# Kernel tuning notes

Hardware: AMD Instinct MI355X
Metric: run time of the kernel (lower is better)

Reference implementation:

```python
import jax, jax.numpy as jnp
import numpy as np

N, E = 50000, 600000
IN_DIM, HID, OUT_DIM = 128, 256, 64


def _sage_conv(x, edge_index, W_l, W_r, b):
    # PyG SAGEConv (mean aggr, root_weight=True):
    # out = mean_{j in N(i)} x_j @ W_l + x_i @ W_r + b
    src, dst = edge_index[0], edge_index[1]
    msg = x[src]  # [E, d] gather
    agg = jax.ops.segment_sum(msg, dst, num_segments=N)  # [N, d]
    cnt = jax.ops.segment_sum(jnp.ones((E,), dtype=x.dtype), dst, num_segments=N)
    agg = agg / jnp.maximum(cnt, 1.0)[:, None]
    return agg @ W_l + x @ W_r + b


def setup_inputs() -> dict:
    key = jax.random.key(0)
    ks = jax.random.split(key, 8)
    x = jax.random.normal(ks[0], (N, IN_DIM), dtype=jnp.float32)
    edge_index = jax.random.randint(ks[1], (2, E), 0, N, dtype=jnp.int64)
    s1 = 1.0 / np.sqrt(IN_DIM)
    s2 = 1.0 / np.sqrt(HID)
    W1_l = jax.random.uniform(ks[2], (IN_DIM, HID), jnp.float32, -s1, s1)
    W1_r = jax.random.uniform(ks[3], (IN_DIM, HID), jnp.float32, -s1, s1)
    b1 = jnp.zeros((HID,), jnp.float32)
    W2_l = jax.random.uniform(ks[4], (HID, OUT_DIM), jnp.float32, -s2, s2)
    W2_r = jax.random.uniform(ks[5], (HID, OUT_DIM), jnp.float32, -s2, s2)
    b2 = jnp.zeros((OUT_DIM,), jnp.float32)
    return {"x": x, "edge_index": edge_index, "W1_l": W1_l, "W1_r": W1_r,
            "b1": b1, "W2_l": W2_l, "W2_r": W2_r, "b2": b2}


def reference(x, edge_index, W1_l, W1_r, b1, W2_l, W2_r, b2):
    # SAGE.forward, eval mode (dropout = identity)
    h = jax.nn.relu(_sage_conv(x, edge_index, W1_l, W1_r, b1))
    out = _sage_conv(h, edge_index, W2_l, W2_r, b2)
    return out
```

## Files before the change

### kernel.cpp

```cpp
#include <hip/hip_runtime.h>

#define N_NODES 50000
#define N_EDGES 600000
#define N_PAD   50048
#define IN_DIM 128
#define HID 256
#define OUT_DIM 64
#define MAX_DEG 64

typedef __attribute__((ext_vector_type(4))) float f32x4;
typedef __attribute__((ext_vector_type(8))) short short8;
typedef unsigned short u16;
typedef unsigned int u32;

__device__ __forceinline__ float bf2f(u32 lo16) {
  u32 u = lo16 << 16;
  return __builtin_bit_cast(float, u);
}
__device__ __forceinline__ u16 f2bf(float f) {
  u32 u = __builtin_bit_cast(u32, f);
  u = (u + 0x7FFF + ((u >> 16) & 1)) >> 16;
  return (u16)u;
}

#define SEG0 (N_PAD * 16)
#define SEG1 (SEG0 + 128 * 64)
#define SEG2 (SEG1 + 64 * 64)
#define SEG3 (SEG2 + N_NODES)
#define PREP_TOT SEG3

__global__ void k_prep(const float* __restrict__ x,
                       const float* __restrict__ W1l, const float* __restrict__ W1r,
                       const float* __restrict__ W2l, const float* __restrict__ W2r,
                       u16* __restrict__ xb, u16* __restrict__ W1p,
                       u16* __restrict__ W2p, int* __restrict__ cnt) {
  int idx = blockIdx.x * 256 + threadIdx.x;
  if (idx < SEG0) {
    int row = idx >> 4;
    int c8 = (idx & 15) * 8;
    short8 o;
    if (row < N_NODES) {
      f32x4 a = *(const f32x4*)&x[(size_t)row * 128 + c8];
      f32x4 b = *(const f32x4*)&x[(size_t)row * 128 + c8 + 4];
      o[0] = (short)f2bf(a[0]); o[1] = (short)f2bf(a[1]);
      o[2] = (short)f2bf(a[2]); o[3] = (short)f2bf(a[3]);
      o[4] = (short)f2bf(b[0]); o[5] = (short)f2bf(b[1]);
      o[6] = (short)f2bf(b[2]); o[7] = (short)f2bf(b[3]);
    } else {
      for (int j = 0; j < 8; ++j) o[j] = 0;
    }
    *(short8*)&xb[(size_t)row * 128 + c8] = o;
  } else if (idx < SEG1) {
    int i = idx - SEG0;
    int F = i >> 6, l = i & 63;
    int wch = F >> 6, kt = (F >> 4) & 3, kk = (F >> 3) & 1, n = F & 7;
    int row = wch * 128 + n * 16 + (l & 15);
    int kb = kt * 64 + kk * 32 + (l >> 4) * 8;
    short8 o;
#pragma unroll
    for (int j = 0; j < 8; ++j) {
      int k = kb + j;
      float v = (k < 128) ? W1l[(size_t)k * HID + row] : W1r[(size_t)(k - 128) * HID + row];
      o[j] = (short)f2bf(v);
    }
    *(short8*)&W1p[(size_t)i * 8] = o;
  } else if (idx < SEG2) {
    int i = idx - SEG1;
    int G = i >> 6, l = i & 63;
    int wch = G >> 5, kk = (G >> 2) & 7, n = G & 3;
    int row = wch * 64 + n * 16 + (l & 15);
    int kb = kk * 32 + (l >> 4) * 8;
    short8 o;
#pragma unroll
    for (int j = 0; j < 8; ++j) {
      int k = kb + j;
      float v = (row < 64) ? W2l[(size_t)k * OUT_DIM + row]
                           : W2r[(size_t)k * OUT_DIM + (row - 64)];
      o[j] = (short)f2bf(v);
    }
    *(short8*)&W2p[(size_t)i * 8] = o;
  } else if (idx < SEG3) {
    cnt[idx - SEG2] = 0;
  }
}


__global__ void k_fill(const int* __restrict__ src, const int* __restrict__ dst,
                       int* __restrict__ cnt, int* __restrict__ bucket) {
  int e = blockIdx.x * 256 + threadIdx.x;
  if (e < N_EDGES) {
    int d = dst[e];
    int pos = atomicAdd(&cnt[d], 1);
    if (pos < MAX_DEG) bucket[(size_t)d * MAX_DEG + pos] = src[e];
  }
}


__global__ void k_agg(const u16* __restrict__ xb, const int* __restrict__ cnt,
                      const int* __restrict__ bucket, u16* __restrict__ agg) {
  int node = blockIdx.x * 4 + (threadIdx.x >> 6);
  if (node >= N_PAD) return;
  int lane = threadIdx.x & 63;
  int es = lane >> 4, dl = lane & 15;
  int deg = (node < N_NODES) ? cnt[node] : 0;
  int sreg = (node < N_NODES) ? bucket[(size_t)node * MAX_DEG + lane] : 0;
  float acc[8] = {0.f, 0.f, 0.f, 0.f, 0.f, 0.f, 0.f, 0.f};
  short8 pend = (short8){0, 0, 0, 0, 0, 0, 0, 0};
  for (int e = 0; e < deg; e += 4) {
    int ee = e + es;
    int s = __shfl(sreg, ee & 63);
    short8 v = (short8){0, 0, 0, 0, 0, 0, 0, 0};
    if (ee < deg) v = *(const short8*)&xb[(size_t)s * 128 + dl * 8];
#pragma unroll
    for (int j = 0; j < 8; ++j) acc[j] += bf2f((u16)pend[j]);
    pend = v;
  }
#pragma unroll
  for (int j = 0; j < 8; ++j) acc[j] += bf2f((u16)pend[j]);
#pragma unroll
  for (int j = 0; j < 8; ++j) {
    acc[j] += __shfl_xor(acc[j], 16);
    acc[j] += __shfl_xor(acc[j], 32);
  }
  float inv = 1.f / fmaxf((float)deg, 1.f);
  if (es == 0) {
    short8 o;
#pragma unroll
    for (int j = 0; j < 8; ++j) o[j] = (short)f2bf(acc[j] * inv);
    *(short8*)&agg[(size_t)node * 128 + dl * 8] = o;
  }
}


__device__ __forceinline__ void gl_lds16(const void* g, void* l) {
  __builtin_amdgcn_global_load_lds((const __attribute__((address_space(1))) u32*)g,
                                   (__attribute__((address_space(3))) u32*)l, 16, 0, 0);
}

__global__ __launch_bounds__(256, 3) void k_mlp(
    const u16* __restrict__ agg, const u16* __restrict__ xb,
    const u16* __restrict__ W1p, const u16* __restrict__ W2p,
    const float* __restrict__ b1, u16* __restrict__ pb, u16* __restrict__ qb) {
  __shared__ u16 hs[64 * 256];
  __shared__ u16 As[2][64 * 64];
  const int t = threadIdx.x;
  const int wave = t >> 6;
  const int lane = t & 63;
  const int brow = blockIdx.x * 64;
  const int lr = lane & 15;
  const int kg = lane >> 4;
  const int wch = wave & 1;

  const int wr = (wave >> 1) * 32;
  const int wc = wch * 128;

  f32x4 acc[2][8];
#pragma unroll
  for (int m = 0; m < 2; ++m)
#pragma unroll
    for (int n = 0; n < 8; ++n) acc[m][n] = (f32x4){0.f, 0.f, 0.f, 0.f};

  auto stageA = [&](int buf, int kt) {
    const u16* base = (kt < 2) ? agg : xb;
    const int koff = (kt & 1) * 64;
#pragma unroll
    for (int i = 0; i < 2; ++i) {
      int chunk = wave * 2 + i;
      int f = chunk * 1024 + lane * 16;
      int row = f >> 7;
      int cbs = (f & 127) ^ ((row & 7) << 4);
      gl_lds16(&base[(size_t)(brow + row) * 128 + koff + (cbs >> 1)],
               (char*)As[buf] + chunk * 1024);
    }
  };

  stageA(0, 0);
  __syncthreads();

#pragma unroll
  for (int kt = 0; kt < 4; ++kt) {
    const int cur = kt & 1;
    if (kt < 3) stageA(cur ^ 1, kt + 1);
#pragma unroll
    for (int kk = 0; kk < 2; ++kk) {
      short8 af[2], bfr[8];
      const int cb = kk * 64 + kg * 16;
#pragma unroll
      for (int m = 0; m < 2; ++m) {
        int row = wr + m * 16 + lr;
        af[m] = *(const short8*)((const char*)As[cur] + row * 128 + (cb ^ ((row & 7) << 4)));
      }
#pragma unroll
      for (int n = 0; n < 8; ++n)
        bfr[n] = *(const short8*)&W1p[(size_t)(((wch * 4 + kt) * 2 + kk) * 8 + n) * 512 +
                                      lane * 8];
#pragma unroll
      for (int m = 0; m < 2; ++m)
#pragma unroll
        for (int n = 0; n < 8; ++n)
          acc[m][n] =
              __builtin_amdgcn_mfma_f32_16x16x32_bf16(af[m], bfr[n], acc[m][n], 0, 0, 0);
    }
    __syncthreads();
  }

#pragma unroll
  for (int n = 0; n < 8; ++n) {
    int col = wc + n * 16 + lr;
    float bv = b1[col];
#pragma unroll
    for (int m = 0; m < 2; ++m) {
#pragma unroll
      for (int j = 0; j < 4; ++j) {
        int row = wr + kg * 4 + m * 16 + j;
        float v = fmaxf(acc[m][n][j] + bv, 0.f);
        *(u16*)((char*)hs + row * 512 + ((col * 2) ^ ((row & 7) << 4))) = f2bf(v);
      }
    }
  }
  __syncthreads();

  const int wr2 = (wave >> 1) * 32;
  f32x4 acc2[2][4];
#pragma unroll
  for (int m = 0; m < 2; ++m)
#pragma unroll
    for (int n = 0; n < 4; ++n) acc2[m][n] = (f32x4){0.f, 0.f, 0.f, 0.f};

#pragma unroll
  for (int kk = 0; kk < 8; ++kk) {
    const int cb = kk * 64 + kg * 16;
    short8 af[2], bfr[4];
#pragma unroll
    for (int m = 0; m < 2; ++m) {
      int row = wr2 + m * 16 + lr;
      af[m] = *(const short8*)((const char*)hs + row * 512 + (cb ^ ((row & 7) << 4)));
    }
#pragma unroll
    for (int n = 0; n < 4; ++n)
      bfr[n] = *(const short8*)&W2p[(size_t)((wch * 8 + kk) * 4 + n) * 512 + lane * 8];
#pragma unroll
    for (int m = 0; m < 2; ++m)
#pragma unroll
      for (int n = 0; n < 4; ++n)
        acc2[m][n] =
            __builtin_amdgcn_mfma_f32_16x16x32_bf16(af[m], bfr[n], acc2[m][n], 0, 0, 0);
  }

  u16* outb = wch ? qb : pb;
#pragma unroll
  for (int n = 0; n < 4; ++n) {
    int col = n * 16 + lr;
#pragma unroll
    for (int m = 0; m < 2; ++m) {
#pragma unroll
      for (int j = 0; j < 4; ++j) {
        int row = brow + wr2 + kg * 4 + m * 16 + j;
        outb[(size_t)row * 64 + col] = f2bf(acc2[m][n][j]);
      }
    }
  }
}


__global__ void k_out(const u16* __restrict__ pb, const u16* __restrict__ qb,
                      const int* __restrict__ cnt, const int* __restrict__ bucket,
                      const float* __restrict__ b2, float* __restrict__ out) {
  int node = blockIdx.x * 4 + (threadIdx.x >> 6);
  if (node >= N_NODES) return;
  int lane = threadIdx.x & 63;
  int es = lane >> 3, dl = lane & 7;
  int deg = cnt[node];
  int sreg = bucket[(size_t)node * MAX_DEG + lane];
  float acc[8] = {0.f, 0.f, 0.f, 0.f, 0.f, 0.f, 0.f, 0.f};
  short8 pend = (short8){0, 0, 0, 0, 0, 0, 0, 0};
  for (int e = 0; e < deg; e += 8) {
    int ee = e + es;
    int s = __shfl(sreg, ee & 63);
    short8 v = (short8){0, 0, 0, 0, 0, 0, 0, 0};
    if (ee < deg) v = *(const short8*)&pb[(size_t)s * 64 + dl * 8];
#pragma unroll
    for (int j = 0; j < 8; ++j) acc[j] += bf2f((u16)pend[j]);
    pend = v;
  }
#pragma unroll
  for (int j = 0; j < 8; ++j) acc[j] += bf2f((u16)pend[j]);
#pragma unroll
  for (int j = 0; j < 8; ++j) {
    acc[j] += __shfl_xor(acc[j], 8);
    acc[j] += __shfl_xor(acc[j], 16);
    acc[j] += __shfl_xor(acc[j], 32);
  }
  float inv = 1.f / fmaxf((float)deg, 1.f);
  if (es == 0) {
    short8 q = *(const short8*)&qb[(size_t)node * 64 + dl * 8];
    f32x4 bb0 = *(const f32x4*)&b2[dl * 8];
    f32x4 bb1 = *(const f32x4*)&b2[dl * 8 + 4];
    f32x4 o0, o1;
#pragma unroll
    for (int j = 0; j < 4; ++j) {
      o0[j] = acc[j] * inv + bf2f((u16)q[j]) + bb0[j];
      o1[j] = acc[j + 4] * inv + bf2f((u16)q[j + 4]) + bb1[j];
    }
    *(f32x4*)&out[(size_t)node * 64 + dl * 8] = o0;
    *(f32x4*)&out[(size_t)node * 64 + dl * 8 + 4] = o1;
  }
}


extern "C" void kernel_launch(void* const* d_in, const int* in_sizes, int n_in,
                              void* d_out, int out_size, void* d_ws, size_t ws_size,
                              hipStream_t stream) {
  const float* x   = (const float*)d_in[0];
  const int*   ei  = (const int*)d_in[1];
  const float* W1l = (const float*)d_in[2];
  const float* W1r = (const float*)d_in[3];
  const float* b1  = (const float*)d_in[4];
  const float* W2l = (const float*)d_in[5];
  const float* W2r = (const float*)d_in[6];
  const float* b2  = (const float*)d_in[7];
  float* out = (float*)d_out;

  const int* src = ei;
  const int* dst = ei + N_EDGES;

  char* ws = (char*)d_ws;
  size_t off = 0;
  auto alloc = [&](size_t bytes) -> void* {
    void* p = ws + off;
    off = (off + bytes + 255) & ~(size_t)255;
    return p;
  };
  int* cnt    = (int*)alloc((size_t)N_NODES * 4);
  int* bucket = (int*)alloc((size_t)N_NODES * MAX_DEG * 4);
  u16* xb     = (u16*)alloc((size_t)N_PAD * 128 * 2);
  u16* agg    = (u16*)alloc((size_t)N_PAD * 128 * 2);
  u16* W1p    = (u16*)alloc((size_t)128 * 64 * 8 * 2);
  u16* W2p    = (u16*)alloc((size_t)64 * 64 * 8 * 2);
  u16* pb     = (u16*)alloc((size_t)N_PAD * 64 * 2);
  u16* qb     = (u16*)alloc((size_t)N_PAD * 64 * 2);

  k_prep<<<(PREP_TOT + 255) / 256, 256, 0, stream>>>(x, W1l, W1r, W2l, W2r,
                                                     xb, W1p, W2p, cnt);
  k_fill<<<(N_EDGES + 255) / 256, 256, 0, stream>>>(src, dst, cnt, bucket);
  k_agg<<<N_PAD / 4, 256, 0, stream>>>(xb, cnt, bucket, agg);
  k_mlp<<<N_PAD / 64, 256, 0, stream>>>(agg, xb, W1p, W2p, b1, pb, qb);
  k_out<<<(N_NODES + 3) / 4, 256, 0, stream>>>(pb, qb, cnt, bucket, b2, out);
}
```

Measured before the change: 112.4 us.

## Fuse bucket fill into prep kernel with XCD-partitioned destination ranges and u16 bucket

```diff
diff --git a/kernel.cpp b/kernel.cpp
--- a/kernel.cpp
+++ b/kernel.cpp
@@ -7,6 +7,9 @@
 #define HID 256
 #define OUT_DIM 64
 #define MAX_DEG 64
+#define NODES_PER_XCD 6250
+#define NF 1024
+#define CHUNK 2048
 
 typedef __attribute__((ext_vector_type(4))) float f32x4;
 typedef __attribute__((ext_vector_type(8))) short short8;
@@ -26,15 +29,56 @@
 #define SEG0 (N_PAD * 16)
 #define SEG1 (SEG0 + 128 * 64)
 #define SEG2 (SEG1 + 64 * 64)
-#define SEG3 (SEG2 + N_NODES)
-#define PREP_TOT SEG3
-
-__global__ void k_prep(const float* __restrict__ x,
-                       const float* __restrict__ W1l, const float* __restrict__ W1r,
-                       const float* __restrict__ W2l, const float* __restrict__ W2r,
-                       u16* __restrict__ xb, u16* __restrict__ W1p,
-                       u16* __restrict__ W2p, int* __restrict__ cnt) {
-  int idx = blockIdx.x * 256 + threadIdx.x;
+#define PREP_TOT SEG2
+
+__global__ void k_prep_fill(const float* __restrict__ x,
+                            const float* __restrict__ W1l, const float* __restrict__ W1r,
+                            const float* __restrict__ W2l, const float* __restrict__ W2r,
+                            const int* __restrict__ src, const int* __restrict__ dst,
+                            u16* __restrict__ xb, u16* __restrict__ W1p,
+                            u16* __restrict__ W2p, int* __restrict__ cnt,
+                            u16* __restrict__ bucket, int* __restrict__ cur) {
+  if (blockIdx.x < NF) {
+    int xcc;
+    asm volatile("s_getreg_b32 %0, hwreg(HW_REG_XCC_ID)" : "=s"(xcc));
+    xcc &= 15;
+    const int lo = xcc * NODES_PER_XCD, hi = lo + NODES_PER_XCD;
+    const int t = threadIdx.x;
+    __shared__ int cbase;
+    for (;;) {
+      __syncthreads();
+      if (t == 0) cbase = atomicAdd(&cur[xcc], CHUNK);
+      __syncthreads();
+      int c = cbase;
+      if (c >= N_EDGES) break;
+#pragma unroll
+      for (int p = 0; p < CHUNK / 1024; ++p) {
+        int e0 = c + p * 1024 + t * 4;
+        if (e0 < N_EDGES) {
+          int4 s4 = *(const int4*)&src[e0];
+          int4 d4 = *(const int4*)&dst[e0];
+          if (d4.x >= lo && d4.x < hi) {
+            int pos = atomicAdd(&cnt[d4.x], 1);
+            if (pos < MAX_DEG) bucket[(size_t)d4.x * MAX_DEG + pos] = (u16)s4.x;
+          }
+          if (d4.y >= lo && d4.y < hi) {
+            int pos = atomicAdd(&cnt[d4.y], 1);
+            if (pos < MAX_DEG) bucket[(size_t)d4.y * MAX_DEG + pos] = (u16)s4.y;
+          }
+          if (d4.z >= lo && d4.z < hi) {
+            int pos = atomicAdd(&cnt[d4.z], 1);
+            if (pos < MAX_DEG) bucket[(size_t)d4.z * MAX_DEG + pos] = (u16)s4.z;
+          }
+          if (d4.w >= lo && d4.w < hi) {
+            int pos = atomicAdd(&cnt[d4.w], 1);
+            if (pos < MAX_DEG) bucket[(size_t)d4.w * MAX_DEG + pos] = (u16)s4.w;
+          }
+        }
+      }
+    }
+    return;
+  }
+  int idx = (blockIdx.x - NF) * 256 + threadIdx.x;
   if (idx < SEG0) {
     int row = idx >> 4;
     int c8 = (idx & 15) * 8;
@@ -79,31 +123,18 @@
       o[j] = (short)f2bf(v);
     }
     *(short8*)&W2p[(size_t)i * 8] = o;
-  } else if (idx < SEG3) {
-    cnt[idx - SEG2] = 0;
-  }
-}
-
-
-__global__ void k_fill(const int* __restrict__ src, const int* __restrict__ dst,
-                       int* __restrict__ cnt, int* __restrict__ bucket) {
-  int e = blockIdx.x * 256 + threadIdx.x;
-  if (e < N_EDGES) {
-    int d = dst[e];
-    int pos = atomicAdd(&cnt[d], 1);
-    if (pos < MAX_DEG) bucket[(size_t)d * MAX_DEG + pos] = src[e];
   }
 }
 
 
 __global__ void k_agg(const u16* __restrict__ xb, const int* __restrict__ cnt,
-                      const int* __restrict__ bucket, u16* __restrict__ agg) {
+                      const u16* __restrict__ bucket, u16* __restrict__ agg) {
   int node = blockIdx.x * 4 + (threadIdx.x >> 6);
   if (node >= N_PAD) return;
   int lane = threadIdx.x & 63;
   int es = lane >> 4, dl = lane & 15;
   int deg = (node < N_NODES) ? cnt[node] : 0;
-  int sreg = (node < N_NODES) ? bucket[(size_t)node * MAX_DEG + lane] : 0;
+  int sreg = (node < N_NODES) ? (int)bucket[(size_t)node * MAX_DEG + lane] : 0;
   float acc[8] = {0.f, 0.f, 0.f, 0.f, 0.f, 0.f, 0.f, 0.f};
   short8 pend = (short8){0, 0, 0, 0, 0, 0, 0, 0};
   for (int e = 0; e < deg; e += 4) {
@@ -264,14 +295,14 @@
 
 
 __global__ void k_out(const u16* __restrict__ pb, const u16* __restrict__ qb,
-                      const int* __restrict__ cnt, const int* __restrict__ bucket,
+                      const int* __restrict__ cnt, const u16* __restrict__ bucket,
                       const float* __restrict__ b2, float* __restrict__ out) {
   int node = blockIdx.x * 4 + (threadIdx.x >> 6);
   if (node >= N_NODES) return;
   int lane = threadIdx.x & 63;
   int es = lane >> 3, dl = lane & 7;
   int deg = cnt[node];
-  int sreg = bucket[(size_t)node * MAX_DEG + lane];
+  int sreg = (int)bucket[(size_t)node * MAX_DEG + lane];
   float acc[8] = {0.f, 0.f, 0.f, 0.f, 0.f, 0.f, 0.f, 0.f};
   short8 pend = (short8){0, 0, 0, 0, 0, 0, 0, 0};
   for (int e = 0; e < deg; e += 8) {
@@ -332,7 +363,9 @@
     return p;
   };
   int* cnt    = (int*)alloc((size_t)N_NODES * 4);
-  int* bucket = (int*)alloc((size_t)N_NODES * MAX_DEG * 4);
+  int* cur    = (int*)alloc(16 * 4);
+  size_t zero_span = off;
+  u16* bucket = (u16*)alloc((size_t)N_NODES * MAX_DEG * 2);
   u16* xb     = (u16*)alloc((size_t)N_PAD * 128 * 2);
   u16* agg    = (u16*)alloc((size_t)N_PAD * 128 * 2);
   u16* W1p    = (u16*)alloc((size_t)128 * 64 * 8 * 2);
@@ -340,9 +373,11 @@
   u16* pb     = (u16*)alloc((size_t)N_PAD * 64 * 2);
   u16* qb     = (u16*)alloc((size_t)N_PAD * 64 * 2);
 
-  k_prep<<<(PREP_TOT + 255) / 256, 256, 0, stream>>>(x, W1l, W1r, W2l, W2r,
-                                                     xb, W1p, W2p, cnt);
-  k_fill<<<(N_EDGES + 255) / 256, 256, 0, stream>>>(src, dst, cnt, bucket);
+  hipMemsetAsync(ws, 0, zero_span, stream);
+
+  int prep_blocks = NF + (PREP_TOT + 255) / 256;
+  k_prep_fill<<<prep_blocks, 256, 0, stream>>>(x, W1l, W1r, W2l, W2r, src, dst,
+                                               xb, W1p, W2p, cnt, bucket, cur);
   k_agg<<<N_PAD / 4, 256, 0, stream>>>(xb, cnt, bucket, agg);
   k_mlp<<<N_PAD / 64, 256, 0, stream>>>(agg, xb, W1p, W2p, b1, pb, qb);
   k_out<<<(N_NODES + 3) / 4, 256, 0, stream>>>(pb, qb, cnt, bucket, b2, out);
```

Result: slower. 134.1 us (+19.3%).

## Build neighbor buckets via two-pass binned partition with LDS atomics and 16-bit indices

Applied to the files above, without the earlier changes.

```diff
diff --git a/kernel.cpp b/kernel.cpp
--- a/kernel.cpp
+++ b/kernel.cpp
@@ -7,6 +7,10 @@
 #define HID 256
 #define OUT_DIM 64
 #define MAX_DEG 64
+#define NBINS 196
+#define BCAP 4096
+#define NPART 256
+#define ECHUNK 2344
 
 typedef __attribute__((ext_vector_type(4))) float f32x4;
 typedef __attribute__((ext_vector_type(8))) short short8;
@@ -26,15 +30,38 @@
 #define SEG0 (N_PAD * 16)
 #define SEG1 (SEG0 + 128 * 64)
 #define SEG2 (SEG1 + 64 * 64)
-#define SEG3 (SEG2 + N_NODES)
-#define PREP_TOT SEG3
-
-__global__ void k_prep(const float* __restrict__ x,
-                       const float* __restrict__ W1l, const float* __restrict__ W1r,
-                       const float* __restrict__ W2l, const float* __restrict__ W2r,
-                       u16* __restrict__ xb, u16* __restrict__ W1p,
-                       u16* __restrict__ W2p, int* __restrict__ cnt) {
-  int idx = blockIdx.x * 256 + threadIdx.x;
+#define PREP_TOT SEG2
+
+__global__ void k_prep_part(const float* __restrict__ x,
+                            const float* __restrict__ W1l, const float* __restrict__ W1r,
+                            const float* __restrict__ W2l, const float* __restrict__ W2r,
+                            const int* __restrict__ src, const int* __restrict__ dst,
+                            u16* __restrict__ xb, u16* __restrict__ W1p,
+                            u16* __restrict__ W2p, u32* __restrict__ region,
+                            int* __restrict__ gcur) {
+  if (blockIdx.x < NPART) {
+    __shared__ int hist[256];
+    __shared__ int base[256];
+    const int t = threadIdx.x;
+    hist[t] = 0;
+    __syncthreads();
+    const int e0 = blockIdx.x * ECHUNK;
+    const int e1 = min(e0 + ECHUNK, N_EDGES);
+    for (int e = e0 + t; e < e1; e += 256) atomicAdd(&hist[dst[e] >> 8], 1);
+    __syncthreads();
+    base[t] = (hist[t] > 0) ? atomicAdd(&gcur[t], hist[t]) : 0;
+    hist[t] = 0;
+    __syncthreads();
+    for (int e = e0 + t; e < e1; e += 256) {
+      int d = dst[e];
+      int bin = d >> 8;
+      int idx = base[bin] + atomicAdd(&hist[bin], 1);
+      if (idx < BCAP)
+        region[(size_t)bin * BCAP + idx] = (u32)(src[e] & 0xffff) | ((u32)(d & 255) << 16);
+    }
+    return;
+  }
+  int idx = (blockIdx.x - NPART) * 256 + threadIdx.x;
   if (idx < SEG0) {
     int row = idx >> 4;
     int c8 = (idx & 15) * 8;
@@ -79,31 +106,48 @@
       o[j] = (short)f2bf(v);
     }
     *(short8*)&W2p[(size_t)i * 8] = o;
-  } else if (idx < SEG3) {
-    cnt[idx - SEG2] = 0;
-  }
-}
-
-
-__global__ void k_fill(const int* __restrict__ src, const int* __restrict__ dst,
-                       int* __restrict__ cnt, int* __restrict__ bucket) {
-  int e = blockIdx.x * 256 + threadIdx.x;
-  if (e < N_EDGES) {
-    int d = dst[e];
-    int pos = atomicAdd(&cnt[d], 1);
-    if (pos < MAX_DEG) bucket[(size_t)d * MAX_DEG + pos] = src[e];
+  }
+}
+
+
+__global__ __launch_bounds__(256) void k_build(const u32* __restrict__ region,
+                                               const int* __restrict__ gcur,
+                                               int* __restrict__ cnt,
+                                               u16* __restrict__ bucket) {
+  __shared__ u16 lbkt[256 * 64];
+  __shared__ int lcnt[256];
+  const int t = threadIdx.x;
+  const int bin = blockIdx.x;
+  lcnt[t] = 0;
+  __syncthreads();
+  int n = gcur[bin];
+  if (n > BCAP) n = BCAP;
+  for (int i = t; i < n; i += 256) {
+    u32 r = region[(size_t)bin * BCAP + i];
+    int dl = (r >> 16) & 255;
+    int pos = atomicAdd(&lcnt[dl], 1);
+    if (pos < MAX_DEG) lbkt[dl * 64 + pos] = (u16)(r & 0xffff);
+  }
+  __syncthreads();
+  int gnode = bin * 256 + t;
+  if (gnode < N_NODES) cnt[gnode] = lcnt[t];
+  for (int i = t; i < 2048; i += 256) {
+    int nl = i >> 3, sub = i & 7;
+    int gn = bin * 256 + nl;
+    if (gn < N_NODES)
+      *(short8*)&bucket[(size_t)gn * 64 + sub * 8] = *(const short8*)&lbkt[nl * 64 + sub * 8];
   }
 }
 
 
 __global__ void k_agg(const u16* __restrict__ xb, const int* __restrict__ cnt,
-                      const int* __restrict__ bucket, u16* __restrict__ agg) {
+                      const u16* __restrict__ bucket, u16* __restrict__ agg) {
   int node = blockIdx.x * 4 + (threadIdx.x >> 6);
   if (node >= N_PAD) return;
   int lane = threadIdx.x & 63;
   int es = lane >> 4, dl = lane & 15;
   int deg = (node < N_NODES) ? cnt[node] : 0;
-  int sreg = (node < N_NODES) ? bucket[(size_t)node * MAX_DEG + lane] : 0;
+  int sreg = (node < N_NODES) ? (int)bucket[(size_t)node * MAX_DEG + lane] : 0;
   float acc[8] = {0.f, 0.f, 0.f, 0.f, 0.f, 0.f, 0.f, 0.f};
   short8 pend = (short8){0, 0, 0, 0, 0, 0, 0, 0};
   for (int e = 0; e < deg; e += 4) {
@@ -264,14 +308,14 @@
 
 
 __global__ void k_out(const u16* __restrict__ pb, const u16* __restrict__ qb,
-                      const int* __restrict__ cnt, const int* __restrict__ bucket,
+                      const int* __restrict__ cnt, const u16* __restrict__ bucket,
                       const float* __restrict__ b2, float* __restrict__ out) {
   int node = blockIdx.x * 4 + (threadIdx.x >> 6);
   if (node >= N_NODES) return;
   int lane = threadIdx.x & 63;
   int es = lane >> 3, dl = lane & 7;
   int deg = cnt[node];
-  int sreg = bucket[(size_t)node * MAX_DEG + lane];
+  int sreg = (int)bucket[(size_t)node * MAX_DEG + lane];
   float acc[8] = {0.f, 0.f, 0.f, 0.f, 0.f, 0.f, 0.f, 0.f};
   short8 pend = (short8){0, 0, 0, 0, 0, 0, 0, 0};
   for (int e = 0; e < deg; e += 8) {
@@ -331,8 +375,10 @@
     off = (off + bytes + 255) & ~(size_t)255;
     return p;
   };
+  int* gcur   = (int*)alloc(256 * 4);
+  u32* region = (u32*)alloc((size_t)NBINS * BCAP * 4);
   int* cnt    = (int*)alloc((size_t)N_NODES * 4);
-  int* bucket = (int*)alloc((size_t)N_NODES * MAX_DEG * 4);
+  u16* bucket = (u16*)alloc((size_t)N_NODES * MAX_DEG * 2);
   u16* xb     = (u16*)alloc((size_t)N_PAD * 128 * 2);
   u16* agg    = (u16*)alloc((size_t)N_PAD * 128 * 2);
   u16* W1p    = (u16*)alloc((size_t)128 * 64 * 8 * 2);
@@ -340,9 +386,12 @@
   u16* pb     = (u16*)alloc((size_t)N_PAD * 64 * 2);
   u16* qb     = (u16*)alloc((size_t)N_PAD * 64 * 2);
 
-  k_prep<<<(PREP_TOT + 255) / 256, 256, 0, stream>>>(x, W1l, W1r, W2l, W2r,
-                                                     xb, W1p, W2p, cnt);
-  k_fill<<<(N_EDGES + 255) / 256, 256, 0, stream>>>(src, dst, cnt, bucket);
+  hipMemsetAsync(gcur, 0, 256 * 4, stream);
+
+  int blocks = NPART + (PREP_TOT + 255) / 256;
+  k_prep_part<<<blocks, 256, 0, stream>>>(x, W1l, W1r, W2l, W2r, src, dst,
+                                          xb, W1p, W2p, region, gcur);
+  k_build<<<NBINS, 256, 0, stream>>>(region, gcur, cnt, bucket);
   k_agg<<<N_PAD / 4, 256, 0, stream>>>(xb, cnt, bucket, agg);
   k_mlp<<<N_PAD / 64, 256, 0, stream>>>(agg, xb, W1p, W2p, b1, pb, qb);
   k_out<<<(N_NODES + 3) / 4, 256, 0, stream>>>(pb, qb, cnt, bucket, b2, out);
```

After: 102.2 us. 9.1% less time.
